# Kernel optimization log

Measured on AMD Instinct MI355X. Metric: run time of the kernel, lower is better.

Reference implementation:

```python
import jax, jax.numpy as jnp
import numpy as np

EMB = 1024
FFN = 4096
H = 16
HD = EMB // H
EPS = 1e-6
SLOPE = 0.01


def leaky_relu(x):
    return jnp.where(x >= 0, x, SLOPE * x)


def layer_norm(x, g, b):
    mu = jnp.mean(x, axis=-1, keepdims=True)
    var = jnp.mean((x - mu) ** 2, axis=-1, keepdims=True)
    return (x - mu) * jax.lax.rsqrt(var + EPS) * g + b


def setup_inputs() -> dict:
    key = jax.random.key(0)
    ks = jax.random.split(key, 16)
    B, N = 2, 2048
    x = jax.random.normal(ks[0], (B, N, EMB), dtype=jnp.float32)

    def lin(k, fan_in, fan_out, kaiming_normal):
        kw, kb = jax.random.split(k)
        gain = float(np.sqrt(2.0 / (1.0 + SLOPE ** 2)))
        if kaiming_normal:
            W = jax.random.normal(kw, (fan_out, fan_in)) * (gain / np.sqrt(fan_in))
        else:
            bound = gain * np.sqrt(3.0 / fan_in)
            W = jax.random.uniform(kw, (fan_out, fan_in), minval=-bound, maxval=bound)
        b = jax.random.normal(kb, (fan_out,)) * 1e-6
        return W.astype(jnp.float32), b.astype(jnp.float32)

    Wq, bq = lin(ks[1], EMB, EMB, True)
    Wk, bk = lin(ks[2], EMB, EMB, True)
    Wv, bv = lin(ks[3], EMB, EMB, True)
    Wo, bo = lin(ks[4], EMB, EMB, True)
    W1, b1 = lin(ks[5], EMB, FFN, False)
    W2, b2 = lin(ks[6], FFN, EMB, False)
    return {
        "x": x,
        "ln1_g": jnp.ones((EMB,)), "ln1_b": jnp.zeros((EMB,)),
        "ln2_g": jnp.ones((EMB,)), "ln2_b": jnp.zeros((EMB,)),
        "Wq": Wq, "bq": bq, "Wk": Wk, "bk": bk, "Wv": Wv, "bv": bv,
        "Wo": Wo, "bo": bo, "W1": W1, "b1": b1, "W2": W2, "b2": b2,
    }


def reference(x, ln1_g, ln1_b, ln2_g, ln2_b, Wq, bq, Wk, bk, Wv, bv, Wo, bo, W1, b1, W2, b2):
    B, N, _ = x.shape
    h = x
    xn = layer_norm(x, ln1_g, ln1_b)
    # QKV projections, split heads: [B, H, N, HD]
    def heads(t):
        return t.reshape(B, N, H, HD).transpose(0, 2, 1, 3)
    q = heads(xn @ Wq.T + bq)
    k = heads(xn @ Wk.T + bk)
    v = heads(xn @ Wv.T + bv)
    scores = jnp.einsum('bhnd,bhmd->bhnm', q, k) / jnp.sqrt(jnp.float32(HD))
    probs = leaky_relu(scores)  # non-softmax attention
    ctx = jnp.einsum('bhnm,bhmd->bhnd', probs, v)
    ctx = ctx.transpose(0, 2, 1, 3).reshape(B, N, EMB)
    attn_out = ctx @ Wo.T + bo
    x = attn_out + h
    h = x
    xn = layer_norm(x, ln2_g, ln2_b)
    ff = leaky_relu(xn @ W1.T + b1) @ W2.T + b2
    return ff + h
```

## Files before the change

### kernel.cpp

```cpp
#include <hip/hip_runtime.h>
#include <hip/hip_bf16.h>


typedef unsigned short u16;
typedef unsigned int u32;
typedef __bf16 bf16x8 __attribute__((ext_vector_type(8)));
typedef __bf16 bf16x4 __attribute__((ext_vector_type(4)));
typedef float f32x4 __attribute__((ext_vector_type(4)));
typedef unsigned short u16x8 __attribute__((ext_vector_type(8)));
typedef unsigned int u32x2 __attribute__((ext_vector_type(2)));
typedef short s16x4 __attribute__((ext_vector_type(4)));

typedef const __attribute__((address_space(1))) void* as1cv;
typedef __attribute__((address_space(3))) void* as3v;

#define MFMA16(a, b, c) __builtin_amdgcn_mfma_f32_16x16x32_bf16((a), (b), (c), 0, 0, 0)
#define GLL16(g, l) __builtin_amdgcn_global_load_lds((as1cv)(g), (as3v)(l), 16, 0, 0)

__device__ __forceinline__ u16 f2bf(float f) {
  unsigned u = __builtin_bit_cast(unsigned, f);
  u += 0x7fffu + ((u >> 16) & 1u);
  return (u16)(u >> 16);
}
__device__ __forceinline__ float bf2f(u16 u) {
  return __builtin_bit_cast(float, ((unsigned)u) << 16);
}
__device__ __forceinline__ float lrelu(float v) { return fmaxf(v, 0.01f * v); }

__device__ __forceinline__ void mfma16x16(f32x4& c, bf16x4 a, bf16x4 b) {
#if __has_builtin(__builtin_amdgcn_mfma_f32_16x16x16bf16_1k)
  c = __builtin_amdgcn_mfma_f32_16x16x16bf16_1k(
      __builtin_bit_cast(s16x4, a), __builtin_bit_cast(s16x4, b), c, 0, 0, 0);
#else
  u32x2 au = __builtin_bit_cast(u32x2, a);
  u32x2 bu = __builtin_bit_cast(u32x2, b);
  asm volatile("s_nop 2\n\tv_mfma_f32_16x16x16_bf16 %0, %1, %2, %0"
               : "+v"(c) : "v"(au), "v"(bu));
#endif
}

__device__ __forceinline__ int xcds(int bid, int nwg) {
  int cpx = nwg >> 3;
  return (bid & 7) * cpx + (bid >> 3);
}

__global__ __launch_bounds__(256) void cvt6(
    const float* __restrict__ p0, const float* __restrict__ p1,
    const float* __restrict__ p2, const float* __restrict__ p3,
    const float* __restrict__ p4, const float* __restrict__ p5,
    u16* __restrict__ o0, u16* __restrict__ o1, u16* __restrict__ o2,
    u16* __restrict__ o3, u16* __restrict__ o4, u16* __restrict__ o5)
{
  int i = blockIdx.x * 256 + threadIdx.x;
  const float* src; u16* dst; int off;
  if (i < 4 * 131072) {
    int s = i >> 17; off = i & 131071;
    src = (s == 0) ? p0 : (s == 1) ? p1 : (s == 2) ? p2 : p3;
    dst = (s == 0) ? o0 : (s == 1) ? o1 : (s == 2) ? o2 : o3;
  } else {
    int j = i - 4 * 131072;
    int s = j >> 19; off = j & 524287;
    src = s ? p5 : p4;
    dst = s ? o5 : o4;
  }
  const float4* s4 = (const float4*)src;
  float4 a = s4[(size_t)off * 2], b = s4[(size_t)off * 2 + 1];
  u16x8 o = { f2bf(a.x), f2bf(a.y), f2bf(a.z), f2bf(a.w),
              f2bf(b.x), f2bf(b.y), f2bf(b.z), f2bf(b.w) };
  *(u16x8*)(dst + (size_t)off * 8) = o;
}

__global__ __launch_bounds__(256) void ln_k(
    const float* __restrict__ x, const float* __restrict__ g,
    const float* __restrict__ bb, u16* __restrict__ out)
{
  const int tid = threadIdx.x;
  const int row = blockIdx.x;
  const float4* xr = (const float4*)(x + (size_t)row * 1024);
  float4 v = xr[tid];
  float s  = v.x + v.y + v.z + v.w;
  float s2 = v.x*v.x + v.y*v.y + v.z*v.z + v.w*v.w;
#pragma unroll
  for (int o = 32; o > 0; o >>= 1) { s += __shfl_down(s, o, 64); s2 += __shfl_down(s2, o, 64); }
  __shared__ float sh[8];
  if ((tid & 63) == 0) { sh[tid >> 6] = s; sh[4 + (tid >> 6)] = s2; }
  __syncthreads();
  s  = sh[0] + sh[1] + sh[2] + sh[3];
  s2 = sh[4] + sh[5] + sh[6] + sh[7];
  float mu  = s * (1.0f / 1024.0f);
  float var = s2 * (1.0f / 1024.0f) - mu * mu;
  float rs  = rsqrtf(var + 1e-6f);
  float4 gv = ((const float4*)g)[tid];
  float4 bv = ((const float4*)bb)[tid];
  ushort4 o;
  o.x = f2bf((v.x - mu) * rs * gv.x + bv.x);
  o.y = f2bf((v.y - mu) * rs * gv.y + bv.y);
  o.z = f2bf((v.z - mu) * rs * gv.z + bv.z);
  o.w = f2bf((v.w - mu) * rs * gv.w + bv.w);
  ((ushort4*)out)[(size_t)row * 256 + tid] = o;
}

__device__ __forceinline__ void gemm_core128(
    const u16* __restrict__ A, const u16* __restrict__ W,
    int kstride, int klen,
    int row0, int wrow0, u16* lsA, u16* lsB, f32x4 (&acc)[4][4])
{
  const int tid  = threadIdx.x;
  const int lane = tid & 63, wave = tid >> 6;
  const int wr = wave >> 1, wc = wave & 1;
  const int lr = lane & 15, lg = lane >> 4;

  const int srow = tid >> 3;
  const int sg   = (tid & 7) ^ (srow & 7);
  const u16* ga0 = A + (size_t)(row0 +  0 + srow) * kstride + sg * 8;
  const u16* ga1 = A + (size_t)(row0 + 32 + srow) * kstride + sg * 8;
  const u16* ga2 = A + (size_t)(row0 + 64 + srow) * kstride + sg * 8;
  const u16* ga3 = A + (size_t)(row0 + 96 + srow) * kstride + sg * 8;
  const u16* gb0 = W + (size_t)(wrow0 +  0 + srow) * kstride + sg * 8;
  const u16* gb1 = W + (size_t)(wrow0 + 32 + srow) * kstride + sg * 8;
  const u16* gb2 = W + (size_t)(wrow0 + 64 + srow) * kstride + sg * 8;
  const u16* gb3 = W + (size_t)(wrow0 + 96 + srow) * kstride + sg * 8;
  u16* la = lsA + tid * 8;
  u16* lb = lsB + tid * 8;

#define GSTAGE(buf)                                                   \
  {                                                                   \
    GLL16(ga0, la + (buf) * 8192 + 0 * 2048);                         \
    GLL16(ga1, la + (buf) * 8192 + 1 * 2048);                         \
    GLL16(ga2, la + (buf) * 8192 + 2 * 2048);                         \
    GLL16(ga3, la + (buf) * 8192 + 3 * 2048);                         \
    GLL16(gb0, lb + (buf) * 8192 + 0 * 2048);                         \
    GLL16(gb1, lb + (buf) * 8192 + 1 * 2048);                         \
    GLL16(gb2, lb + (buf) * 8192 + 2 * 2048);                         \
    GLL16(gb3, lb + (buf) * 8192 + 3 * 2048);                         \
    ga0 += 64; ga1 += 64; ga2 += 64; ga3 += 64;                       \
    gb0 += 64; gb1 += 64; gb2 += 64; gb3 += 64;                       \
  }

  const int nsteps = klen >> 6;
  GSTAGE(0); GSTAGE(1);

  const int swzr = lr & 7;
  for (int t = 0; t < nsteps; t++) {
    if (t + 1 < nsteps) asm volatile("s_waitcnt vmcnt(8)" ::: "memory");
    else                asm volatile("s_waitcnt vmcnt(0)" ::: "memory");
    __builtin_amdgcn_s_barrier();
    asm volatile("" ::: "memory");

    const u16* cA = lsA + (t & 1) * 8192;
    const u16* cB = lsB + (t & 1) * 8192;
#pragma unroll
    for (int ks = 0; ks < 2; ks++) {
      bf16x8 av[4], bv[4];
#pragma unroll
      for (int mi = 0; mi < 4; mi++)
        av[mi] = *reinterpret_cast<const bf16x8*>(
            cA + (wr * 64 + mi * 16 + lr) * 64 + (((ks * 4 + lg) ^ swzr) * 8));
#pragma unroll
      for (int ni = 0; ni < 4; ni++)
        bv[ni] = *reinterpret_cast<const bf16x8*>(
            cB + (wc * 64 + ni * 16 + lr) * 64 + (((ks * 4 + lg) ^ swzr) * 8));
#pragma unroll
      for (int mi = 0; mi < 4; mi++)
#pragma unroll
        for (int ni = 0; ni < 4; ni++)
          acc[mi][ni] = MFMA16(av[mi], bv[ni], acc[mi][ni]);
    }

    __builtin_amdgcn_s_barrier();
    asm volatile("" ::: "memory");
    if (t + 2 < nsteps) GSTAGE(t & 1);
  }
#undef GSTAGE
}

__global__ __launch_bounds__(256, 2) void gemm_qkv(
    const u16* __restrict__ xn,
    const u16* __restrict__ Wq, const u16* __restrict__ Wk, const u16* __restrict__ Wv,
    const float* __restrict__ bq, const float* __restrict__ bk, const float* __restrict__ bv,
    u16* __restrict__ qb, u16* __restrict__ kb, u16* __restrict__ vtb)
{
  __shared__ u16 lsA[2 * 8192];
  __shared__ u16 lsB[2 * 8192];
  const int wid = xcds(blockIdx.x, 768);
  const int mt = wid / 24, nt = wid % 24;
  const int row0 = mt * 128, col0 = nt * 128;
  const int sel = col0 >> 10, c0 = col0 & 1023;
  const u16* W = (sel == 0) ? Wq : (sel == 1) ? Wk : Wv;
  const float* bias = (sel == 0) ? bq : (sel == 1) ? bk : bv;

  f32x4 acc[4][4];
  f32x4 z = {0.f, 0.f, 0.f, 0.f};
#pragma unroll
  for (int mi = 0; mi < 4; mi++)
#pragma unroll
    for (int ni = 0; ni < 4; ni++) acc[mi][ni] = z;

  gemm_core128(xn, W, 1024, 1024, row0, c0, lsA, lsB, acc);

  const int lane = threadIdx.x & 63, wave = threadIdx.x >> 6;
  const int wr = wave >> 1, wc = wave & 1;
  const int lr = lane & 15, lg = lane >> 4;
  const float qscale = (sel == 0) ? 0.125f : 1.0f;
#pragma unroll
  for (int ni = 0; ni < 4; ni++) {
    int c = c0 + wc * 64 + ni * 16 + lr;
    float bsv = bias[c];
    int h = c >> 6, hd = c & 63;
#pragma unroll
    for (int mi = 0; mi < 4; mi++) {
      int rbase = row0 + wr * 64 + mi * 16 + lg * 4;
      int b = rbase >> 11;
      int n = rbase & 2047;
      if (sel < 2) {
        u16* dst = (sel == 0) ? qb : kb;
        size_t base = ((size_t)(b * 16 + h) * 2048 + n) * 64 + hd;
#pragma unroll
        for (int r = 0; r < 4; r++)
          dst[base + (size_t)r * 64] = f2bf((acc[mi][ni][r] + bsv) * qscale);
      } else {
        size_t base = ((size_t)((b * 16 + h) * 64 + hd)) * 2048 + n;
        ushort4 o;
        o.x = f2bf(acc[mi][ni][0] + bsv);
        o.y = f2bf(acc[mi][ni][1] + bsv);
        o.z = f2bf(acc[mi][ni][2] + bsv);
        o.w = f2bf(acc[mi][ni][3] + bsv);
        *(ushort4*)(vtb + base) = o;
      }
    }
  }
}

template <int EPI>
__global__ __launch_bounds__(256, 2) void gemm128(
    const u16* __restrict__ A, const u16* __restrict__ W,
    const float* __restrict__ bias, float* __restrict__ outf,
    u16* __restrict__ outh, const float* __restrict__ extra,
    int K, int nTiles, int nwg)
{
  __shared__ u16 lsA[2 * 8192];
  __shared__ u16 lsB[2 * 8192];
  const int wid = xcds(blockIdx.x, nwg);
  const int mt = wid / nTiles, nt = wid % nTiles;
  const int row0 = mt * 128, col0 = nt * 128;

  f32x4 acc[4][4];
  f32x4 z = {0.f, 0.f, 0.f, 0.f};
#pragma unroll
  for (int mi = 0; mi < 4; mi++)
#pragma unroll
    for (int ni = 0; ni < 4; ni++) acc[mi][ni] = z;

  gemm_core128(A, W, K, K, row0, col0, lsA, lsB, acc);

  const int N = nTiles * 128;
  const int lane = threadIdx.x & 63, wave = threadIdx.x >> 6;
  const int wr = wave >> 1, wc = wave & 1;
  const int lr = lane & 15, lg = lane >> 4;
#pragma unroll
  for (int ni = 0; ni < 4; ni++) {
    int col = col0 + wc * 64 + ni * 16 + lr;
    float bsv = bias[col];
#pragma unroll
    for (int mi = 0; mi < 4; mi++) {
      int rbase = row0 + wr * 64 + mi * 16 + lg * 4;
#pragma unroll
      for (int r = 0; r < 4; r++) {
        float v = acc[mi][ni][r] + bsv;
        size_t idx = (size_t)(rbase + r) * N + col;
        if (EPI == 0) {
          outf[idx] = v + extra[idx];
        } else {
          outh[idx] = f2bf(lrelu(v));
        }
      }
    }
  }
}

__global__ __launch_bounds__(256, 2) void gemm_ffn2(
    const u16* __restrict__ A, const u16* __restrict__ W,
    u16* __restrict__ pout)
{
  __shared__ u16 lsA[2 * 8192];
  __shared__ u16 lsB[2 * 8192];
  const int wid = xcds(blockIdx.x, 1024);
  const int chunk = wid >> 8, rem = wid & 255;
  const int mt = rem >> 3, nt = rem & 7;
  const int row0 = mt * 128, col0 = nt * 128;

  f32x4 acc[4][4];
  f32x4 z = {0.f, 0.f, 0.f, 0.f};
#pragma unroll
  for (int mi = 0; mi < 4; mi++)
#pragma unroll
    for (int ni = 0; ni < 4; ni++) acc[mi][ni] = z;

  gemm_core128(A + chunk * 1024, W + chunk * 1024, 4096, 1024,
               row0, col0, lsA, lsB, acc);

  u16* out = pout + (size_t)chunk * (4096 * 1024);
  const int lane = threadIdx.x & 63, wave = threadIdx.x >> 6;
  const int wr = wave >> 1, wc = wave & 1;
  const int lr = lane & 15, lg = lane >> 4;
#pragma unroll
  for (int ni = 0; ni < 4; ni++) {
    int col = col0 + wc * 64 + ni * 16 + lr;
#pragma unroll
    for (int mi = 0; mi < 4; mi++) {
      int rbase = row0 + wr * 64 + mi * 16 + lg * 4;
#pragma unroll
      for (int r = 0; r < 4; r++)
        out[(size_t)(rbase + r) * 1024 + col] = f2bf(acc[mi][ni][r]);
    }
  }
}

__global__ __launch_bounds__(256) void reduce_ffn2(
    const u16* __restrict__ p, const float* __restrict__ b2,
    const float* __restrict__ x2, float* __restrict__ out)
{
  size_t i = ((size_t)blockIdx.x * 256 + threadIdx.x) * 4;
  int col = (int)(i & 1023);
  ushort4 a0 = *(const ushort4*)(p + i);
  ushort4 a1 = *(const ushort4*)(p + (size_t)(4096 * 1024) + i);
  ushort4 a2 = *(const ushort4*)(p + (size_t)(2 * 4096 * 1024) + i);
  ushort4 a3 = *(const ushort4*)(p + (size_t)(3 * 4096 * 1024) + i);
  float4 bv = *(const float4*)(b2 + col);
  float4 xv = *(const float4*)(x2 + i);
  float4 r;
  r.x = bf2f(a0.x) + bf2f(a1.x) + bf2f(a2.x) + bf2f(a3.x) + bv.x + xv.x;
  r.y = bf2f(a0.y) + bf2f(a1.y) + bf2f(a2.y) + bf2f(a3.y) + bv.y + xv.y;
  r.z = bf2f(a0.z) + bf2f(a1.z) + bf2f(a2.z) + bf2f(a3.z) + bv.z + xv.z;
  r.w = bf2f(a0.w) + bf2f(a1.w) + bf2f(a2.w) + bf2f(a3.w) + bv.w + xv.w;
  *(float4*)(out + i) = r;
}

__global__ __launch_bounds__(256, 3) void attn_k(
    const u16* __restrict__ qb, const u16* __restrict__ kb,
    const u16* __restrict__ vtb, u16* __restrict__ ctx)
{
  __shared__ u16 lds[3 * 8192];

  const int tid = threadIdx.x;
  const int lane = tid & 63, wq = tid >> 6;
  const int lr = lane & 15, lg = lane >> 4;
  const int wid = xcds(blockIdx.x, 512);
  const int bh = wid >> 4, qt = wid & 15;
  const int n0 = qt * 128;
  const u16* qh = qb + (size_t)bh * 2048 * 64;
  const u16* kh = kb + (size_t)bh * 2048 * 64;
  const u16* vh = vtb + (size_t)bh * 64 * 2048;

  const int srow = tid >> 3;
  const int sgg  = (tid & 7) ^ (srow & 7);
  const size_t koff0 = (size_t)srow * 64 + sgg * 8;
  const size_t koff1 = koff0 + (size_t)32 * 64;
  const size_t voff0 = (size_t)srow * 2048 + sgg * 8;
  const size_t voff1 = voff0 + (size_t)32 * 2048;
  const int dk0 = tid * 8, dk1 = tid * 8 + 2048;

#define STAGE_KV(t, jb)                                              \
  {                                                                  \
    const u16* ks_ = kh + (size_t)(t) * 4096;                        \
    const u16* vs_ = vh + (t) * 64;                                  \
    u16* lb_ = lds + (jb) * 8192;                                    \
    GLL16(ks_ + koff0, lb_ + dk0);                                   \
    GLL16(ks_ + koff1, lb_ + dk1);                                   \
    GLL16(vs_ + voff0, lb_ + 4096 + dk0);                            \
    GLL16(vs_ + voff1, lb_ + 4096 + dk1);                            \
  }

  STAGE_KV(0, 0);
  STAGE_KV(1, 1);

  bf16x8 qr[2][2];
#pragma unroll
  for (int qi = 0; qi < 2; qi++)
#pragma unroll
    for (int ks = 0; ks < 2; ks++)
      qr[qi][ks] = *(const bf16x8*)(
          qh + (size_t)(n0 + wq * 32 + qi * 16 + lr) * 64 + ks * 32 + lg * 8);
  asm volatile("" ::: "memory");

  f32x4 z = {0.f, 0.f, 0.f, 0.f};
  f32x4 cacc[4][2];
#pragma unroll
  for (int di = 0; di < 4; di++) { cacc[di][0] = z; cacc[di][1] = z; }

  const int lswz = lr & 7;
  int bi = 0, bs = 2;
  for (int t = 0; t < 32; t++) {
    if (t < 31) asm volatile("s_waitcnt vmcnt(4)" ::: "memory");
    else        asm volatile("s_waitcnt vmcnt(0)" ::: "memory");
    __builtin_amdgcn_s_barrier();
    asm volatile("" ::: "memory");
    if (t + 2 < 32) { STAGE_KV(t + 2, bs); bs = (bs == 2) ? 0 : bs + 1; }

    const u16* lk = lds + bi * 8192;
    const u16* lv = lds + bi * 8192 + 4096;
#pragma unroll
    for (int ki = 0; ki < 4; ki++) {
      f32x4 s0 = z, s1 = z;
#pragma unroll
      for (int ks = 0; ks < 2; ks++) {
        bf16x8 kf = *(const bf16x8*)(
            lk + (ki * 16 + lr) * 64 + (((ks * 4 + lg) ^ lswz) * 8));
        s0 = MFMA16(kf, qr[0][ks], s0);
        s1 = MFMA16(kf, qr[1][ks], s1);
      }
      bf16x4 p0, p1;
#pragma unroll
      for (int r = 0; r < 4; r++) {
        p0[r] = (__bf16)lrelu(s0[r]);
        p1[r] = (__bf16)lrelu(s1[r]);
      }
#pragma unroll
      for (int di = 0; di < 4; di++) {
        bf16x4 vf = *(const bf16x4*)(
            lv + (di * 16 + lr) * 64 +
            (((ki * 2 + (lg >> 1)) ^ lswz) * 8) + (lg & 1) * 4);
        mfma16x16(cacc[di][0], vf, p0);
        mfma16x16(cacc[di][1], vf, p1);
      }
    }
    bi = (bi == 2) ? 0 : bi + 1;
  }

  const int b = bh >> 4, h = bh & 15;
#pragma unroll
  for (int qi = 0; qi < 2; qi++) {
    int n = n0 + wq * 32 + qi * 16 + lr;
    u16* op = ctx + ((size_t)(b * 2048 + n)) * 1024 + h * 64;
#pragma unroll
    for (int di = 0; di < 4; di++) {
      ushort4 o;
      o.x = f2bf(cacc[di][qi][0]);
      o.y = f2bf(cacc[di][qi][1]);
      o.z = f2bf(cacc[di][qi][2]);
      o.w = f2bf(cacc[di][qi][3]);
      *(ushort4*)(op + di * 16 + lg * 4) = o;
    }
  }
#undef STAGE_KV
}

extern "C" void kernel_launch(void* const* d_in, const int* in_sizes, int n_in,
                              void* d_out, int out_size, void* d_ws, size_t ws_size,
                              hipStream_t stream) {
  (void)in_sizes; (void)n_in; (void)out_size; (void)ws_size;
  const float* x    = (const float*)d_in[0];
  const float* ln1g = (const float*)d_in[1];
  const float* ln1b = (const float*)d_in[2];
  const float* ln2g = (const float*)d_in[3];
  const float* ln2b = (const float*)d_in[4];
  const float* Wq = (const float*)d_in[5];  const float* bq = (const float*)d_in[6];
  const float* Wk = (const float*)d_in[7];  const float* bk = (const float*)d_in[8];
  const float* Wv = (const float*)d_in[9];  const float* bv = (const float*)d_in[10];
  const float* Wo = (const float*)d_in[11]; const float* bo = (const float*)d_in[12];
  const float* W1 = (const float*)d_in[13]; const float* b1 = (const float*)d_in[14];
  const float* W2 = (const float*)d_in[15]; const float* b2 = (const float*)d_in[16];

  char* ws = (char*)d_ws;
  u16*   WqB  = (u16*)(ws + ((size_t)0 << 20));
  u16*   WkB  = (u16*)(ws + ((size_t)2 << 20));
  u16*   WvB  = (u16*)(ws + ((size_t)4 << 20));
  u16*   WoB  = (u16*)(ws + ((size_t)6 << 20));
  u16*   W1B  = (u16*)(ws + ((size_t)8 << 20));
  u16*   W2B  = (u16*)(ws + ((size_t)16 << 20));
  u16*   xn1  = (u16*)(ws + ((size_t)24 << 20));
  u16*   qb   = (u16*)(ws + ((size_t)32 << 20));
  u16*   kb   = (u16*)(ws + ((size_t)40 << 20));
  u16*   vtb  = (u16*)(ws + ((size_t)48 << 20));
  u16*   ctxb = (u16*)(ws + ((size_t)56 << 20));
  float* x2   = (float*)(ws + ((size_t)64 << 20));
  u16*   xn2  = (u16*)(ws + ((size_t)80 << 20));
  u16*   ff1  = (u16*)(ws + ((size_t)88 << 20));
  u16*   pF2  = (u16*)(ws + ((size_t)24 << 20));

  dim3 blk(256);

  cvt6<<<dim3(6144), blk, 0, stream>>>(Wq, Wk, Wv, Wo, W1, W2,
                                       WqB, WkB, WvB, WoB, W1B, W2B);
  ln_k<<<dim3(4096), blk, 0, stream>>>(x, ln1g, ln1b, xn1);
  gemm_qkv<<<dim3(768), blk, 0, stream>>>(xn1, WqB, WkB, WvB, bq, bk, bv,
                                          qb, kb, vtb);
  attn_k<<<dim3(512), blk, 0, stream>>>(qb, kb, vtb, ctxb);
  gemm128<0><<<dim3(256), blk, 0, stream>>>(ctxb, WoB, bo, x2, (u16*)nullptr, x,
                                            1024, 8, 256);
  ln_k<<<dim3(4096), blk, 0, stream>>>(x2, ln2g, ln2b, xn2);
  gemm128<1><<<dim3(1024), blk, 0, stream>>>(xn2, W1B, b1, (float*)nullptr, ff1,
                                             (const float*)nullptr, 1024, 32, 1024);
  gemm_ffn2<<<dim3(1024), blk, 0, stream>>>(ff1, W2B, pF2);
  reduce_ffn2<<<dim3(4096), blk, 0, stream>>>(pF2, b2, x2, (float*)d_out);
}
```

Before: 333.9 us.

## Use 256x256 tiles with 8-wave blocks for FFN GEMMs

Adds a 256x256-tile GEMM core in which 512-thread blocks each compute a 128x64 sub-tile per wave. It is used for both FFN1 (bias plus leaky-ReLU epilogue) and the split-K FFN2 partials. Each launch shrinks from 1024 small-tile blocks to 256 large-tile blocks, which doubles operand reuse per byte loaded into LDS and halves global traffic for A and W. In exchange each block needs 128KB of LDS and many accumulator registers, so only one block fits per CU. There is also a single wave of blocks across the device, which exposes load latency and tail effects. The Wo GEMM is split out into its own specialized kernel.

```diff
diff --git a/kernel.cpp b/kernel.cpp
--- a/kernel.cpp
+++ b/kernel.cpp
@@ -174,6 +174,128 @@
 #undef GSTAGE
 }
 
+__device__ __forceinline__ void gemm_core256(
+    const u16* __restrict__ A, const u16* __restrict__ W,
+    int kstride, int klen,
+    int row0, int col0, u16* lsA, u16* lsB, f32x4 (&acc)[8][4])
+{
+  const int tid  = threadIdx.x;
+  const int lane = tid & 63, wave = tid >> 6;
+  const int wm = wave >> 2, wn = wave & 3;
+  const int lr = lane & 15, lg = lane >> 4;
+
+  const int srow = tid >> 3;
+  const int sg   = (tid & 7) ^ (srow & 7);
+  const u16* ga0 = A + (size_t)(row0 +   0 + srow) * kstride + sg * 8;
+  const u16* ga1 = A + (size_t)(row0 +  64 + srow) * kstride + sg * 8;
+  const u16* ga2 = A + (size_t)(row0 + 128 + srow) * kstride + sg * 8;
+  const u16* ga3 = A + (size_t)(row0 + 192 + srow) * kstride + sg * 8;
+  const u16* gb0 = W + (size_t)(col0 +   0 + srow) * kstride + sg * 8;
+  const u16* gb1 = W + (size_t)(col0 +  64 + srow) * kstride + sg * 8;
+  const u16* gb2 = W + (size_t)(col0 + 128 + srow) * kstride + sg * 8;
+  const u16* gb3 = W + (size_t)(col0 + 192 + srow) * kstride + sg * 8;
+  u16* la = lsA + tid * 8;
+  u16* lb = lsB + tid * 8;
+
+#define GSTAGE2(buf)                                                  \
+  {                                                                   \
+    GLL16(ga0, la + (buf) * 16384 + 0 * 4096);                        \
+    GLL16(ga1, la + (buf) * 16384 + 1 * 4096);                        \
+    GLL16(ga2, la + (buf) * 16384 + 2 * 4096);                        \
+    GLL16(ga3, la + (buf) * 16384 + 3 * 4096);                        \
+    GLL16(gb0, lb + (buf) * 16384 + 0 * 4096);                        \
+    GLL16(gb1, lb + (buf) * 16384 + 1 * 4096);                        \
+    GLL16(gb2, lb + (buf) * 16384 + 2 * 4096);                        \
+    GLL16(gb3, lb + (buf) * 16384 + 3 * 4096);                        \
+    ga0 += 64; ga1 += 64; ga2 += 64; ga3 += 64;                       \
+    gb0 += 64; gb1 += 64; gb2 += 64; gb3 += 64;                       \
+  }
+
+  const int nsteps = klen >> 6;
+  GSTAGE2(0); GSTAGE2(1);
+
+  const int swzr = lr & 7;
+  for (int t = 0; t < nsteps; t++) {
+    if (t + 1 < nsteps) asm volatile("s_waitcnt vmcnt(8)" ::: "memory");
+    else                asm volatile("s_waitcnt vmcnt(0)" ::: "memory");
+    __builtin_amdgcn_s_barrier();
+    asm volatile("" ::: "memory");
+
+    const u16* cA = lsA + (t & 1) * 16384;
+    const u16* cB = lsB + (t & 1) * 16384;
+#pragma unroll
+    for (int ks = 0; ks < 2; ks++) {
+      bf16x8 av[8], bv[4];
+#pragma unroll
+      for (int mi = 0; mi < 8; mi++)
+        av[mi] = *reinterpret_cast<const bf16x8*>(
+            cA + (wm * 128 + mi * 16 + lr) * 64 + (((ks * 4 + lg) ^ swzr) * 8));
+#pragma unroll
+      for (int ni = 0; ni < 4; ni++)
+        bv[ni] = *reinterpret_cast<const bf16x8*>(
+            cB + (wn * 64 + ni * 16 + lr) * 64 + (((ks * 4 + lg) ^ swzr) * 8));
+#pragma unroll
+      for (int mi = 0; mi < 8; mi++)
+#pragma unroll
+        for (int ni = 0; ni < 4; ni++)
+          acc[mi][ni] = MFMA16(av[mi], bv[ni], acc[mi][ni]);
+    }
+
+    __builtin_amdgcn_s_barrier();
+    asm volatile("" ::: "memory");
+    if (t + 2 < nsteps) GSTAGE2(t & 1);
+  }
+#undef GSTAGE2
+}
+
+template <int EPI>
+__global__ __launch_bounds__(512, 2) void gemm256(
+    const u16* __restrict__ A, const u16* __restrict__ W,
+    const float* __restrict__ bias, u16* __restrict__ outh)
+{
+  __shared__ u16 lsA[2 * 16384];
+  __shared__ u16 lsB[2 * 16384];
+  const int wid = xcds(blockIdx.x, 256);
+  int row0, col0, kstride;
+  if (EPI == 1) {
+    row0 = (wid >> 4) * 256; col0 = (wid & 15) * 256; kstride = 1024;
+  } else {
+    const int chunk = wid >> 6, rem = wid & 63;
+    row0 = (rem >> 2) * 256; col0 = (rem & 3) * 256; kstride = 4096;
+    A += chunk * 1024; W += chunk * 1024;
+    outh += (size_t)chunk * (4096 * 1024);
+  }
+
+  f32x4 acc[8][4];
+  f32x4 z = {0.f, 0.f, 0.f, 0.f};
+#pragma unroll
+  for (int mi = 0; mi < 8; mi++)
+#pragma unroll
+    for (int ni = 0; ni < 4; ni++) acc[mi][ni] = z;
+
+  gemm_core256(A, W, kstride, 1024, row0, col0, lsA, lsB, acc);
+
+  const int lane = threadIdx.x & 63, wave = threadIdx.x >> 6;
+  const int wm = wave >> 2, wn = wave & 3;
+  const int lr = lane & 15, lg = lane >> 4;
+  const int NOUT = (EPI == 1) ? 4096 : 1024;
+#pragma unroll
+  for (int ni = 0; ni < 4; ni++) {
+    int col = col0 + wn * 64 + ni * 16 + lr;
+    float bsv = (EPI == 1) ? bias[col] : 0.f;
+#pragma unroll
+    for (int mi = 0; mi < 8; mi++) {
+      int rbase = row0 + wm * 128 + mi * 16 + lg * 4;
+#pragma unroll
+      for (int r = 0; r < 4; r++) {
+        float v = acc[mi][ni][r] + bsv;
+        if (EPI == 1) outh[(size_t)(rbase + r) * NOUT + col] = f2bf(lrelu(v));
+        else          outh[(size_t)(rbase + r) * NOUT + col] = f2bf(v);
+      }
+    }
+  }
+}
+
 __global__ __launch_bounds__(256, 2) void gemm_qkv(
     const u16* __restrict__ xn,
     const u16* __restrict__ Wq, const u16* __restrict__ Wk, const u16* __restrict__ Wv,
@@ -231,17 +353,15 @@
   }
 }
 
-template <int EPI>
-__global__ __launch_bounds__(256, 2) void gemm128(
+__global__ __launch_bounds__(256, 2) void gemm_wo(
     const u16* __restrict__ A, const u16* __restrict__ W,
     const float* __restrict__ bias, float* __restrict__ outf,
-    u16* __restrict__ outh, const float* __restrict__ extra,
-    int K, int nTiles, int nwg)
+    const float* __restrict__ extra)
 {
   __shared__ u16 lsA[2 * 8192];
   __shared__ u16 lsB[2 * 8192];
-  const int wid = xcds(blockIdx.x, nwg);
-  const int mt = wid / nTiles, nt = wid % nTiles;
+  const int wid = xcds(blockIdx.x, 256);
+  const int mt = wid >> 3, nt = wid & 7;
   const int row0 = mt * 128, col0 = nt * 128;
 
   f32x4 acc[4][4];
@@ -251,9 +371,8 @@
 #pragma unroll
     for (int ni = 0; ni < 4; ni++) acc[mi][ni] = z;
 
-  gemm_core128(A, W, K, K, row0, col0, lsA, lsB, acc);
-
-  const int N = nTiles * 128;
+  gemm_core128(A, W, 1024, 1024, row0, col0, lsA, lsB, acc);
+
   const int lane = threadIdx.x & 63, wave = threadIdx.x >> 6;
   const int wr = wave >> 1, wc = wave & 1;
   const int lr = lane & 15, lg = lane >> 4;
@@ -266,52 +385,9 @@
       int rbase = row0 + wr * 64 + mi * 16 + lg * 4;
 #pragma unroll
       for (int r = 0; r < 4; r++) {
-        float v = acc[mi][ni][r] + bsv;
-        size_t idx = (size_t)(rbase + r) * N + col;
-        if (EPI == 0) {
-          outf[idx] = v + extra[idx];
-        } else {
-          outh[idx] = f2bf(lrelu(v));
-        }
+        size_t idx = (size_t)(rbase + r) * 1024 + col;
+        outf[idx] = acc[mi][ni][r] + bsv + extra[idx];
       }
-    }
-  }
-}
-
-__global__ __launch_bounds__(256, 2) void gemm_ffn2(
-    const u16* __restrict__ A, const u16* __restrict__ W,
-    u16* __restrict__ pout)
-{
-  __shared__ u16 lsA[2 * 8192];
-  __shared__ u16 lsB[2 * 8192];
-  const int wid = xcds(blockIdx.x, 1024);
-  const int chunk = wid >> 8, rem = wid & 255;
-  const int mt = rem >> 3, nt = rem & 7;
-  const int row0 = mt * 128, col0 = nt * 128;
-
-  f32x4 acc[4][4];
-  f32x4 z = {0.f, 0.f, 0.f, 0.f};
-#pragma unroll
-  for (int mi = 0; mi < 4; mi++)
-#pragma unroll
-    for (int ni = 0; ni < 4; ni++) acc[mi][ni] = z;
-
-  gemm_core128(A + chunk * 1024, W + chunk * 1024, 4096, 1024,
-               row0, col0, lsA, lsB, acc);
-
-  u16* out = pout + (size_t)chunk * (4096 * 1024);
-  const int lane = threadIdx.x & 63, wave = threadIdx.x >> 6;
-  const int wr = wave >> 1, wc = wave & 1;
-  const int lr = lane & 15, lg = lane >> 4;
-#pragma unroll
-  for (int ni = 0; ni < 4; ni++) {
-    int col = col0 + wc * 64 + ni * 16 + lr;
-#pragma unroll
-    for (int mi = 0; mi < 4; mi++) {
-      int rbase = row0 + wr * 64 + mi * 16 + lg * 4;
-#pragma unroll
-      for (int r = 0; r < 4; r++)
-        out[(size_t)(rbase + r) * 1024 + col] = f2bf(acc[mi][ni][r]);
     }
   }
 }
@@ -486,11 +562,9 @@
   gemm_qkv<<<dim3(768), blk, 0, stream>>>(xn1, WqB, WkB, WvB, bq, bk, bv,
                                           qb, kb, vtb);
   attn_k<<<dim3(512), blk, 0, stream>>>(qb, kb, vtb, ctxb);
-  gemm128<0><<<dim3(256), blk, 0, stream>>>(ctxb, WoB, bo, x2, (u16*)nullptr, x,
-                                            1024, 8, 256);
+  gemm_wo<<<dim3(256), blk, 0, stream>>>(ctxb, WoB, bo, x2, x);
   ln_k<<<dim3(4096), blk, 0, stream>>>(x2, ln2g, ln2b, xn2);
-  gemm128<1><<<dim3(1024), blk, 0, stream>>>(xn2, W1B, b1, (float*)nullptr, ff1,
-                                             (const float*)nullptr, 1024, 32, 1024);
-  gemm_ffn2<<<dim3(1024), blk, 0, stream>>>(ff1, W2B, pF2);
+  gemm256<1><<<dim3(256), dim3(512), 0, stream>>>(xn2, W1B, b1, ff1);
+  gemm256<2><<<dim3(256), dim3(512), 0, stream>>>(ff1, W2B, (const float*)nullptr, pF2);
   reduce_ffn2<<<dim3(4096), blk, 0, stream>>>(pF2, b2, x2, (float*)d_out);
 }
```

Result: no change. 333.6 us (-0.1%).
